# Kernel optimization log

Hardware: AMD Instinct MI355X
Metric: run time of the kernel (lower is better)

The kernel has to match this reference:

```python
import jax, jax.numpy as jnp
import numpy as np

N_P = 100000; N_F = 100000; N_PORT = 50000
F_IN = 64; H = 128; E = 200000; G = 128; OUT = 2


def setup_inputs() -> dict:
    key = jax.random.key(0)
    it = iter(jax.random.split(key, 64))
    def nrm(sh, s=1.0):
        return jax.random.normal(next(it), sh, jnp.float32) * s
    def ei(ns, nd):
        src = jax.random.randint(next(it), (E,), 0, ns)
        dst = jax.random.randint(next(it), (E,), 0, nd)
        return jnp.stack([src, dst]).astype(jnp.int32)
    def batch(n):
        return jnp.sort(jax.random.randint(next(it), (n,), 0, G)).astype(jnp.int32)
    return {
        'x_process': nrm((N_P, F_IN)), 'x_file': nrm((N_F, F_IN)), 'x_port': nrm((N_PORT, F_IN)),
        'W0': nrm((F_IN, H), 0.1), 'a0s': nrm((H,), 0.1), 'a0d': nrm((H,), 0.1), 'b0': jnp.zeros((H,), jnp.float32),
        'W1': nrm((H, H), 0.1), 'a1s': nrm((H,), 0.1), 'a1d': nrm((H,), 0.1), 'b1': jnp.zeros((H,), jnp.float32),
        'W2': nrm((H, H), 0.1), 'a2s': nrm((H,), 0.1), 'a2d': nrm((H,), 0.1), 'b2': jnp.zeros((H,), jnp.float32),
        'lin1_w': nrm((H, H), 0.1), 'lin1_b': jnp.zeros((H,), jnp.float32),
        'lin2_w': nrm((H, OUT), 0.1), 'lin2_b': jnp.zeros((OUT,), jnp.float32),
        'ei_access': ei(N_P, N_F), 'ei_rev_access': ei(N_F, N_P),
        'ei_same_as': ei(N_P, N_F), 'ei_rev_same_as': ei(N_F, N_P),
        'ei_bind': ei(N_P, N_PORT), 'ei_rev_bind': ei(N_PORT, N_P),
        'ei_session': ei(N_PORT, N_PORT), 'ei_rev_session': ei(N_PORT, N_PORT),
        'ei_create': ei(N_P, N_P), 'ei_rev_create': ei(N_P, N_P),
        'batch_process': batch(N_P), 'batch_file': batch(N_F), 'batch_port': batch(N_PORT),
    }


def _rel(h_src, s_src, d_dst, ei, b, n_dst):
    # single GATConv relation: gather, segment-softmax over dst, scatter-sum
    es, ed = ei[0], ei[1]
    alpha = jax.nn.leaky_relu(s_src[es] + d_dst[ed], 0.2)  # [E]
    m = jax.ops.segment_max(alpha, ed, num_segments=n_dst)
    m = jnp.where(jnp.isfinite(m), m, 0.0)
    ex = jnp.exp(alpha - m[ed])
    den = jax.ops.segment_sum(ex, ed, num_segments=n_dst)
    w = ex / jnp.maximum(den[ed], 1e-16)
    out = jax.ops.segment_sum(w[:, None] * h_src[es], ed, num_segments=n_dst)
    return out + b


def _forward(x_process, x_file, x_port,
             W0, a0s, a0d, b0, W1, a1s, a1d, b1, W2, a2s, a2d, b2,
             lin1_w, lin1_b, lin2_w, lin2_b,
             ei_access, ei_rev_access, ei_same_as, ei_rev_same_as,
             ei_bind, ei_rev_bind, ei_session, ei_rev_session,
             ei_create, ei_rev_create,
             batch_process, batch_file, batch_port):
    xp, xf, xpo = x_process, x_file, x_port
    for W, asr, adr, b in ((W0, a0s, a0d, b0), (W1, a1s, a1d, b1), (W2, a2s, a2d, b2)):
        # shared GATConv weights across all 10 relations -> transform each node type once
        hp, hf, hpo = xp @ W, xf @ W, xpo @ W
        sp, sf, spo = hp @ asr, hf @ asr, hpo @ asr
        dp, df, dpo = hp @ adr, hf @ adr, hpo @ adr
        # HeteroConv(aggr='mean'): average relation outputs per dst node type
        p_new = (_rel(hf, sf, dp, ei_rev_access, b, N_P)
                 + _rel(hf, sf, dp, ei_rev_same_as, b, N_P)
                 + _rel(hpo, spo, dp, ei_rev_bind, b, N_P)
                 + _rel(hp, sp, dp, ei_create, b, N_P)
                 + _rel(hp, sp, dp, ei_rev_create, b, N_P)) / 5.0
        f_new = (_rel(hp, sp, df, ei_access, b, N_F)
                 + _rel(hp, sp, df, ei_same_as, b, N_F)) / 2.0
        po_new = (_rel(hp, sp, dpo, ei_bind, b, N_PORT)
                  + _rel(hpo, spo, dpo, ei_session, b, N_PORT)
                  + _rel(hpo, spo, dpo, ei_rev_session, b, N_PORT)) / 3.0
        xp = jax.nn.leaky_relu(p_new, 0.01)
        xf = jax.nn.leaky_relu(f_new, 0.01)
        xpo = jax.nn.leaky_relu(po_new, 0.01)
    # pool_type == 1: global_add_pool over all node types concatenated
    x = jnp.concatenate([xp, xf, xpo], axis=0)
    bb = jnp.concatenate([batch_process, batch_file, batch_port], axis=0)
    pooled = jax.ops.segment_sum(x, bb, num_segments=G)  # [G, H]
    h = pooled @ lin1_w + lin1_b  # dropout is identity at eval
    return h @ lin2_w + lin2_b  # [G, OUT]


def reference(x_process, x_file, x_port,
              W0, a0s, a0d, b0, W1, a1s, a1d, b1, W2, a2s, a2d, b2,
              lin1_w, lin1_b, lin2_w, lin2_b,
              ei_access, ei_rev_access, ei_same_as, ei_rev_same_as,
              ei_bind, ei_rev_bind, ei_session, ei_rev_session,
              ei_create, ei_rev_create,
              batch_process, batch_file, batch_port):
    return _forward(x_process, x_file, x_port,
                    W0, a0s, a0d, b0, W1, a1s, a1d, b1, W2, a2s, a2d, b2,
                    lin1_w, lin1_b, lin2_w, lin2_b,
                    ei_access, ei_rev_access, ei_same_as, ei_rev_same_as,
                    ei_bind, ei_rev_bind, ei_session, ei_rev_session,
                    ei_create, ei_rev_create,
                    batch_process, batch_file, batch_port)
```

## Files before the change

kernel.cpp:

```cpp
#include <hip/hip_runtime.h>
#include <cstdint>
#include <cstddef>

#define E_EDGES 200000
#define NP 100000
#define NF 100000
#define NPORT 50000
#define NTOT 250000
#define TOTDEG 850000
#define GPOOL 128
#define NPART 8
#define SEGS_PER_PART 106250

typedef __attribute__((ext_vector_type(8))) short bf16x8;
typedef __attribute__((ext_vector_type(4))) float f32x4;

__device__ __forceinline__ float bf2f(unsigned short u) {
    return __uint_as_float(((unsigned int)u) << 16);
}
__device__ __forceinline__ unsigned short f2bf(float f) {
    unsigned int x = __float_as_uint(f);
    return (unsigned short)((x + 0x7fffu + ((x >> 16) & 1u)) >> 16);
}

struct EiPtrs {
    const int* p[10];
};

__device__ __forceinline__ int seg_of(int r, int dst) {
    if (r < 5) return dst * 5 + r;
    if (r < 7) return 500000 + dst * 2 + (r - 5);
    return 700000 + dst * 3 + (r - 7);
}
__device__ __forceinline__ int srcbase_of(int r) {
    return (r <= 1) ? 100000 : (r == 2 || r >= 8) ? 200000 : 0;
}

__global__ __launch_bounds__(256) void k_count_all(EiPtrs eis, int* __restrict__ deg) {
    int r = blockIdx.y;
    int e = blockIdx.x * 256 + threadIdx.x;
    if (e >= E_EDGES) return;
    int seg = seg_of(r, eis.p[r][E_EDGES + e]);
    int lo = blockIdx.z * SEGS_PER_PART;
    if (seg < lo || seg >= lo + SEGS_PER_PART) return;
    atomicAdd(&deg[seg], 1);
}

__global__ __launch_bounds__(256) void k_scan_partial(const int* __restrict__ deg,
                                                      int* __restrict__ bsum) {
    int t = threadIdx.x, b = blockIdx.x;
    int base = b * 1024 + t * 4;
    int sv = 0;
#pragma unroll
    for (int i = 0; i < 4; i++) {
        int idx = base + i;
        if (idx < TOTDEG) sv += deg[idx];
    }
#pragma unroll
    for (int msk = 1; msk < 64; msk <<= 1) sv += __shfl_xor(sv, msk);
    __shared__ int ws[4];
    if ((t & 63) == 0) ws[t >> 6] = sv;
    __syncthreads();
    if (t == 0) bsum[b] = ws[0] + ws[1] + ws[2] + ws[3];
}

__global__ __launch_bounds__(1024) void k_scan_bsums(int* __restrict__ bsum, int nb) {
    __shared__ int lds[1024];
    int t = threadIdx.x;
    int v = (t < nb) ? bsum[t] : 0;
    lds[t] = v;
    __syncthreads();
    for (int dd = 1; dd < 1024; dd <<= 1) {
        int u = (t >= dd) ? lds[t - dd] : 0;
        __syncthreads();
        lds[t] += u;
        __syncthreads();
    }
    if (t < nb) bsum[t] = lds[t] - v;
}

__global__ __launch_bounds__(256) void k_scan_final(const int* __restrict__ deg,
                                                    const int* __restrict__ bsum,
                                                    int* __restrict__ offs) {
    int t = threadIdx.x, b = blockIdx.x;
    int base = b * 1024 + t * 4;
    int v[4];
    int tot = 0;
#pragma unroll
    for (int i = 0; i < 4; i++) {
        int idx = base + i;
        v[i] = (idx < TOTDEG) ? deg[idx] : 0;
        tot += v[i];
    }
    int lane = t & 63, w = t >> 6;
    int x = tot;
#pragma unroll
    for (int dd = 1; dd < 64; dd <<= 1) {
        int u = __shfl_up(x, dd);
        if (lane >= dd) x += u;
    }
    __shared__ int wt[4];
    if (lane == 63) wt[w] = x;
    __syncthreads();
    int wbase = 0;
#pragma unroll
    for (int j = 0; j < 4; j++)
        if (j < w) wbase += wt[j];
    int run = bsum[b] + wbase + (x - tot);
#pragma unroll
    for (int i = 0; i < 4; i++) {
        int idx = base + i;
        if (idx <= TOTDEG) offs[idx] = run;
        run += v[i];
    }
}

__global__ __launch_bounds__(256) void k_fill_all(EiPtrs eis, int* __restrict__ cursor,
                                                  int* __restrict__ list) {
    int r = blockIdx.y;
    int e = blockIdx.x * 256 + threadIdx.x;
    if (e >= E_EDGES) return;
    const int* ei = eis.p[r];
    int seg = seg_of(r, ei[E_EDGES + e]);
    int lo = blockIdx.z * SEGS_PER_PART;
    if (seg < lo || seg >= lo + SEGS_PER_PART) return;
    int pos = atomicAdd(&cursor[seg], 1);
    list[pos] = ei[e] + srcbase_of(r);
}

__global__ __launch_bounds__(256) void k_wt(const float* __restrict__ W,
                                            unsigned short* __restrict__ WT, int K) {
    int idx = blockIdx.x * 256 + threadIdx.x;
    if (idx >= 128 * K) return;
    int col = idx / K, k = idx - col * K;
    WT[idx] = f2bf(W[k * 128 + col]);
}

template <int K, bool BF16IN>
__global__ __launch_bounds__(256) void gemm_mfma(const void* __restrict__ xv,
                                                 const unsigned short* __restrict__ WT,
                                                 const float* __restrict__ avs,
                                                 const float* __restrict__ avd,
                                                 unsigned short* __restrict__ h,
                                                 float* __restrict__ s,
                                                 float* __restrict__ d, int N) {
    constexpr int NQ = K / 32;
    __shared__ float csmem[64][130];
    char* sw = (char*)&csmem[0][0];
    int tid = threadIdx.x;
    int w = tid >> 6, l = tid & 63;
    int row0 = blockIdx.x * 64;

    constexpr int WT_BYTES = 128 * K * 2;
#pragma unroll
    for (int i = tid * 16; i < WT_BYTES; i += 256 * 16) {
        uint4 v = *(const uint4*)((const char*)WT + i);
        int row = i / (2 * K);
        int addr = i ^ ((row & 7) << 4);
        *(uint4*)(sw + addr) = v;
    }

    int arow = row0 + w * 16 + (l & 15);
    bf16x8 afrag[NQ];
    if (arow < N) {
        if (BF16IN) {
            const unsigned short* x = (const unsigned short*)xv;
#pragma unroll
            for (int q = 0; q < NQ; ++q) {
                int kc = q * 32 + (l >> 4) * 8;
                afrag[q] = *(const bf16x8*)&x[(size_t)arow * K + kc];
            }
        } else {
            const float* x = (const float*)xv;
#pragma unroll
            for (int q = 0; q < NQ; ++q) {
                int kc = q * 32 + (l >> 4) * 8;
                float4 f0 = *(const float4*)&x[(size_t)arow * K + kc];
                float4 f1 = *(const float4*)&x[(size_t)arow * K + kc + 4];
                bf16x8 a;
                a[0] = (short)f2bf(f0.x);
                a[1] = (short)f2bf(f0.y);
                a[2] = (short)f2bf(f0.z);
                a[3] = (short)f2bf(f0.w);
                a[4] = (short)f2bf(f1.x);
                a[5] = (short)f2bf(f1.y);
                a[6] = (short)f2bf(f1.z);
                a[7] = (short)f2bf(f1.w);
                afrag[q] = a;
            }
        }
    } else {
#pragma unroll
        for (int q = 0; q < NQ; ++q) {
            bf16x8 z = {0, 0, 0, 0, 0, 0, 0, 0};
            afrag[q] = z;
        }
    }
    __syncthreads();

    f32x4 acc[8];
#pragma unroll
    for (int c = 0; c < 8; ++c) acc[c] = (f32x4){0.f, 0.f, 0.f, 0.f};

#pragma unroll
    for (int c = 0; c < 8; ++c) {
        int cabs = c * 16 + (l & 15);
        int base = cabs * (2 * K) + ((l >> 4) * 16);
        int swz = (cabs & 7) << 4;
#pragma unroll
        for (int q = 0; q < NQ; ++q) {
            int addr = (base + q * 64) ^ swz;
            bf16x8 b = *(const bf16x8*)(sw + addr);
            acc[c] = __builtin_amdgcn_mfma_f32_16x16x32_bf16(afrag[q], b, acc[c], 0, 0, 0);
        }
    }
    __syncthreads();

    int crow = w * 16 + (l >> 4) * 4;
    int ccol = l & 15;
#pragma unroll
    for (int c = 0; c < 8; ++c)
#pragma unroll
        for (int r = 0; r < 4; ++r) csmem[crow + r][c * 16 + ccol] = acc[c][r];
    __syncthreads();

    int row = tid >> 2, cg = tid & 3;
    int grow = row0 + row;
    if (grow < N) {
        float sv = 0.f, dv = 0.f;
        unsigned short tmp[32];
#pragma unroll
        for (int i = 0; i < 32; ++i) {
            float v = csmem[row][cg * 32 + i];
            sv = fmaf(v, avs[cg * 32 + i], sv);
            dv = fmaf(v, avd[cg * 32 + i], dv);
            tmp[i] = f2bf(v);
        }
        unsigned short* hp = &h[(size_t)grow * 128 + cg * 32];
        *(uint4*)&hp[0] = *(uint4*)&tmp[0];
        *(uint4*)&hp[8] = *(uint4*)&tmp[8];
        *(uint4*)&hp[16] = *(uint4*)&tmp[16];
        *(uint4*)&hp[24] = *(uint4*)&tmp[24];
        sv += __shfl_xor(sv, 1);
        sv += __shfl_xor(sv, 2);
        dv += __shfl_xor(dv, 1);
        dv += __shfl_xor(dv, 2);
        if (cg == 0) {
            s[grow] = sv;
            d[grow] = dv;
        }
    }
}

__global__ __launch_bounds__(256) void k_edgew(const int* __restrict__ offs,
                                               const int* __restrict__ list,
                                               const float* __restrict__ s_all,
                                               const float* __restrict__ d_all,
                                               unsigned short* __restrict__ wE) {
    int seg = blockIdx.x * 256 + threadIdx.x;
    if (seg >= TOTDEG) return;
    int o0 = offs[seg], o1 = offs[seg + 1];
    if (o1 == o0) return;
    int dst_g;
    if (seg < 500000)
        dst_g = seg / 5;
    else if (seg < 700000)
        dst_g = 100000 + (seg - 500000) / 2;
    else
        dst_g = 200000 + (seg - 700000) / 3;
    float dd = d_all[dst_g];
    float m = -1e30f, den = 0.f;
    for (int j = o0; j < o1; ++j) {
        float x = s_all[list[j]] + dd;
        x = (x >= 0.f) ? x : 0.2f * x;
        if (x > m) {
            den = den * __expf(m - x) + 1.f;
            m = x;
        } else {
            den += __expf(x - m);
        }
    }
    float invden = 1.f / fmaxf(den, 1e-16f);
    for (int j = o0; j < o1; ++j) {
        float x = s_all[list[j]] + dd;
        x = (x >= 0.f) ? x : 0.2f * x;
        wE[j] = f2bf(__expf(x - m) * invden);
    }
}

__global__ __launch_bounds__(256) void k_gather(const int* __restrict__ offs,
                                                const int* __restrict__ list,
                                                const unsigned short* __restrict__ wE,
                                                const float* __restrict__ bias,
                                                const unsigned short* __restrict__ H,
                                                unsigned short* __restrict__ X) {
    int grp = threadIdx.x >> 5, lane = threadIdx.x & 31;
    int dst = blockIdx.x * 8 + grp;
    if (dst >= NTOT) return;
    int seg0, nrel;
    float inv;
    if (dst < 100000) {
        seg0 = dst * 5;
        nrel = 5;
        inv = 0.2f;
    } else if (dst < 200000) {
        seg0 = 500000 + (dst - 100000) * 2;
        nrel = 2;
        inv = 0.5f;
    } else {
        seg0 = 700000 + (dst - 200000) * 3;
        nrel = 3;
        inv = 1.f / 3.f;
    }
    int o0 = offs[seg0], o1 = offs[seg0 + nrel];
    int half = lane >> 4;
    int l16 = lane & 15;
    float a[8] = {0.f, 0.f, 0.f, 0.f, 0.f, 0.f, 0.f, 0.f};
    float b[8] = {0.f, 0.f, 0.f, 0.f, 0.f, 0.f, 0.f, 0.f};
    int j = o0 + half;
    for (; j + 2 < o1; j += 4) {
        int s0 = list[j], s1 = list[j + 2];
        float w0 = bf2f(wE[j]), w1 = bf2f(wE[j + 2]);
        uint4 r0 = *(const uint4*)&H[(size_t)s0 * 128 + l16 * 8];
        uint4 r1 = *(const uint4*)&H[(size_t)s1 * 128 + l16 * 8];
        const unsigned short* u0 = (const unsigned short*)&r0;
        const unsigned short* u1 = (const unsigned short*)&r1;
#pragma unroll
        for (int k = 0; k < 8; ++k) a[k] = fmaf(w0, bf2f(u0[k]), a[k]);
#pragma unroll
        for (int k = 0; k < 8; ++k) b[k] = fmaf(w1, bf2f(u1[k]), b[k]);
    }
    for (; j < o1; j += 2) {
        int s0 = list[j];
        float w0 = bf2f(wE[j]);
        uint4 r0 = *(const uint4*)&H[(size_t)s0 * 128 + l16 * 8];
        const unsigned short* u0 = (const unsigned short*)&r0;
#pragma unroll
        for (int k = 0; k < 8; ++k) a[k] = fmaf(w0, bf2f(u0[k]), a[k]);
    }
#pragma unroll
    for (int k = 0; k < 8; ++k) {
        a[k] += b[k];
        a[k] += __shfl_xor(a[k], 16);
    }
    int c0 = l16 * 8 + half * 4;
    float4 b4 = *(const float4*)&bias[c0];
    float v0 = fmaf(a[half * 4 + 0], inv, b4.x);
    float v1 = fmaf(a[half * 4 + 1], inv, b4.y);
    float v2 = fmaf(a[half * 4 + 2], inv, b4.z);
    float v3 = fmaf(a[half * 4 + 3], inv, b4.w);
    v0 = (v0 >= 0.f) ? v0 : 0.01f * v0;
    v1 = (v1 >= 0.f) ? v1 : 0.01f * v1;
    v2 = (v2 >= 0.f) ? v2 : 0.01f * v2;
    v3 = (v3 >= 0.f) ? v3 : 0.01f * v3;
    ushort4 o;
    o.x = f2bf(v0);
    o.y = f2bf(v1);
    o.z = f2bf(v2);
    o.w = f2bf(v3);
    *(ushort4*)&X[(size_t)dst * 128 + c0] = o;
}

__global__ __launch_bounds__(128) void pool_all(const unsigned short* __restrict__ X,
                                                const int* __restrict__ bp,
                                                const int* __restrict__ bf,
                                                const int* __restrict__ bpo,
                                                float* __restrict__ pooled) {
    int t = threadIdx.x;
    int start = blockIdx.x * 128;
    int end = min(start + 128, NTOT);
    if (start >= end) return;
    auto bat = [&](int i) {
        return (i < NP) ? bp[i] : (i < NP + NF) ? bf[i - NP] : bpo[i - NP - NF];
    };
    float acc = 0.f;
    int g = bat(start);
    for (int i = start; i < end; ++i) {
        int gi = bat(i);
        if (gi != g) {
            atomicAdd(&pooled[(size_t)g * 128 + t], acc);
            acc = 0.f;
            g = gi;
        }
        acc += bf2f(X[(size_t)i * 128 + t]);
    }
    atomicAdd(&pooled[(size_t)g * 128 + t], acc);
}

__global__ __launch_bounds__(128) void k_mlp(const float* __restrict__ pooled,
                                             const float* __restrict__ w1,
                                             const float* __restrict__ b1,
                                             const float* __restrict__ w2,
                                             const float* __restrict__ b2,
                                             float* __restrict__ out) {
    __shared__ float p[128];
    __shared__ float r0[2], r1[2];
    int g = blockIdx.x, t = threadIdx.x;
    p[t] = pooled[g * 128 + t];
    __syncthreads();
    float acc = b1[t];
    for (int k = 0; k < 128; ++k) acc = fmaf(p[k], w1[k * 128 + t], acc);
    float v0 = acc * w2[t * 2 + 0];
    float v1 = acc * w2[t * 2 + 1];
#pragma unroll
    for (int msk = 1; msk < 64; msk <<= 1) {
        v0 += __shfl_xor(v0, msk);
        v1 += __shfl_xor(v1, msk);
    }
    if ((t & 63) == 0) {
        r0[t >> 6] = v0;
        r1[t >> 6] = v1;
    }
    __syncthreads();
    if (t == 0) {
        out[g * 2 + 0] = r0[0] + r0[1] + b2[0];
        out[g * 2 + 1] = r1[0] + r1[1] + b2[1];
    }
}

__global__ void k_ws_debug(float* out, int n, float val) {
    int i = blockIdx.x * 256 + threadIdx.x;
    if (i < n) out[i] = val;
}

extern "C" void kernel_launch(void* const* d_in, const int* in_sizes, int n_in,
                              void* d_out, int out_size, void* d_ws, size_t ws_size,
                              hipStream_t stream) {
    const float* x_p0 = (const float*)d_in[0];
    const float* x_f0 = (const float*)d_in[1];
    const float* x_po0 = (const float*)d_in[2];
    const float* Wl[3] = {(const float*)d_in[3], (const float*)d_in[7],
                          (const float*)d_in[11]};
    const float* asl[3] = {(const float*)d_in[4], (const float*)d_in[8],
                           (const float*)d_in[12]};
    const float* adl[3] = {(const float*)d_in[5], (const float*)d_in[9],
                           (const float*)d_in[13]};
    const float* bl[3] = {(const float*)d_in[6], (const float*)d_in[10],
                          (const float*)d_in[14]};
    const float* lin1_w = (const float*)d_in[15];
    const float* lin1_b = (const float*)d_in[16];
    const float* lin2_w = (const float*)d_in[17];
    const float* lin2_b = (const float*)d_in[18];
    EiPtrs eis;
    eis.p[0] = (const int*)d_in[20];
    eis.p[1] = (const int*)d_in[22];
    eis.p[2] = (const int*)d_in[24];
    eis.p[3] = (const int*)d_in[27];
    eis.p[4] = (const int*)d_in[28];
    eis.p[5] = (const int*)d_in[19];
    eis.p[6] = (const int*)d_in[21];
    eis.p[7] = (const int*)d_in[23];
    eis.p[8] = (const int*)d_in[25];
    eis.p[9] = (const int*)d_in[26];
    const int* batch_p = (const int*)d_in[29];
    const int* batch_f = (const int*)d_in[30];
    const int* batch_po = (const int*)d_in[31];
    float* out = (float*)d_out;

    char* w = (char*)d_ws;
    size_t off = 0;
    int* offs = (int*)(w + off);      off += (size_t)850004 * 4;
    int* cursor = (int*)(w + off);    off += (size_t)TOTDEG * 4;
    int* list = (int*)(w + off);      off += (size_t)10 * E_EDGES * 4;
    int* bsum = (int*)(w + off);      off += 4096;
    unsigned short* H = (unsigned short*)(w + off); off += (size_t)NTOT * 128 * 2;
    unsigned short* X = (unsigned short*)(w + off); off += (size_t)NTOT * 128 * 2;
    float* s_all = (float*)(w + off); off += (size_t)NTOT * 4;
    float* d_all = (float*)(w + off); off += (size_t)NTOT * 4;
    float* pooled = (float*)(w + off); off += (size_t)GPOOL * 128 * 4;
    unsigned short* WT0 = (unsigned short*)(w + off); off += (size_t)128 * 64 * 2;
    unsigned short* WT1 = (unsigned short*)(w + off); off += (size_t)128 * 128 * 2;
    unsigned short* WT2 = (unsigned short*)(w + off); off += (size_t)128 * 128 * 2;
    unsigned short* wE = (unsigned short*)(w + off); off += (size_t)10 * E_EDGES * 2;
    if (ws_size < off) {
        k_ws_debug<<<(out_size + 255) / 256, 256, 0, stream>>>(out, out_size,
                                                               (float)ws_size);
        return;
    }

    hipMemsetAsync(cursor, 0, (size_t)TOTDEG * 4, stream);
    hipMemsetAsync(pooled, 0, (size_t)GPOOL * 128 * 4, stream);

    k_wt<<<(128 * 64 + 255) / 256, 256, 0, stream>>>(Wl[0], WT0, 64);
    k_wt<<<(128 * 128 + 255) / 256, 256, 0, stream>>>(Wl[1], WT1, 128);
    k_wt<<<(128 * 128 + 255) / 256, 256, 0, stream>>>(Wl[2], WT2, 128);

    int eb = (E_EDGES + 255) / 256;
    k_count_all<<<dim3(eb, 10, NPART), 256, 0, stream>>>(eis, cursor);
    int nb = (TOTDEG + 1 + 1023) / 1024;
    k_scan_partial<<<nb, 256, 0, stream>>>(cursor, bsum);
    k_scan_bsums<<<1, 1024, 0, stream>>>(bsum, nb);
    k_scan_final<<<nb, 256, 0, stream>>>(cursor, bsum, offs);
    hipMemcpyAsync(cursor, offs, (size_t)TOTDEG * 4, hipMemcpyDeviceToDevice, stream);
    k_fill_all<<<dim3(eb, 10, NPART), 256, 0, stream>>>(eis, cursor, list);

    unsigned short* Hp = H;
    unsigned short* Hf = H + (size_t)NP * 128;
    unsigned short* Hpo = H + (size_t)(NP + NF) * 128;
    float* sp_ = s_all;
    float* sf_ = s_all + NP;
    float* spo_ = s_all + NP + NF;
    float* dp_ = d_all;
    float* df_ = d_all + NP;
    float* dpo_ = d_all + NP + NF;

    for (int L = 0; L < 3; ++L) {
        if (L == 0) {
            gemm_mfma<64, false><<<(NP + 63) / 64, 256, 0, stream>>>(
                x_p0, WT0, asl[0], adl[0], Hp, sp_, dp_, NP);
            gemm_mfma<64, false><<<(NF + 63) / 64, 256, 0, stream>>>(
                x_f0, WT0, asl[0], adl[0], Hf, sf_, df_, NF);
            gemm_mfma<64, false><<<(NPORT + 63) / 64, 256, 0, stream>>>(
                x_po0, WT0, asl[0], adl[0], Hpo, spo_, dpo_, NPORT);
        } else {
            const unsigned short* WTL = (L == 1) ? WT1 : WT2;
            gemm_mfma<128, true><<<(NTOT + 63) / 64, 256, 0, stream>>>(
                X, WTL, asl[L], adl[L], H, s_all, d_all, NTOT);
        }
        k_edgew<<<(TOTDEG + 255) / 256, 256, 0, stream>>>(offs, list, s_all, d_all, wE);
        k_gather<<<(NTOT + 7) / 8, 256, 0, stream>>>(offs, list, wE, bl[L], H, X);
    }

    pool_all<<<(NTOT + 127) / 128, 128, 0, stream>>>(X, batch_p, batch_f, batch_po,
                                                     pooled);

    k_mlp<<<GPOOL, 128, 0, stream>>>(pooled, lin1_w, lin1_b, lin2_w, lin2_b, out);
}
```

Before: 862.8 us.

## Fuse edge softmax into gather, merge init kernels and layer-0 GEMM launches

```diff
diff --git a/kernel.cpp b/kernel.cpp
--- a/kernel.cpp
+++ b/kernel.cpp
@@ -9,8 +9,11 @@
 #define NTOT 250000
 #define TOTDEG 850000
 #define GPOOL 128
-#define NPART 8
-#define SEGS_PER_PART 106250
+#define NPART_C 2
+#define SPP_C 425000
+#define NPART_F 4
+#define SPP_F 212500
+#define CAPW 128
 
 typedef __attribute__((ext_vector_type(8))) short bf16x8;
 typedef __attribute__((ext_vector_type(4))) float f32x4;
@@ -34,6 +37,28 @@
 }
 __device__ __forceinline__ int srcbase_of(int r) {
     return (r <= 1) ? 100000 : (r == 2 || r >= 8) ? 200000 : 0;
+}
+
+__global__ __launch_bounds__(256) void k_init(const float* __restrict__ W0,
+                                              const float* __restrict__ W1,
+                                              const float* __restrict__ W2,
+                                              unsigned short* __restrict__ WT0,
+                                              unsigned short* __restrict__ WT1,
+                                              unsigned short* __restrict__ WT2,
+                                              int* __restrict__ cursor,
+                                              float* __restrict__ pooled) {
+    int idx = blockIdx.x * 256 + threadIdx.x;
+    if (idx < TOTDEG) cursor[idx] = 0;
+    if (idx < GPOOL * 128) pooled[idx] = 0.f;
+    if (idx < 128 * 64) {
+        int col = idx / 64, k = idx - col * 64;
+        WT0[idx] = f2bf(W0[k * 128 + col]);
+    }
+    if (idx < 128 * 128) {
+        int col = idx >> 7, k = idx & 127;
+        WT1[idx] = f2bf(W1[k * 128 + col]);
+        WT2[idx] = f2bf(W2[k * 128 + col]);
+    }
 }
 
 __global__ __launch_bounds__(256) void k_count_all(EiPtrs eis, int* __restrict__ deg) {
@@ -41,8 +66,8 @@
     int e = blockIdx.x * 256 + threadIdx.x;
     if (e >= E_EDGES) return;
     int seg = seg_of(r, eis.p[r][E_EDGES + e]);
-    int lo = blockIdx.z * SEGS_PER_PART;
-    if (seg < lo || seg >= lo + SEGS_PER_PART) return;
+    int lo = blockIdx.z * SPP_C;
+    if (seg < lo || seg >= lo + SPP_C) return;
     atomicAdd(&deg[seg], 1);
 }
 
@@ -81,7 +106,8 @@
 
 __global__ __launch_bounds__(256) void k_scan_final(const int* __restrict__ deg,
                                                     const int* __restrict__ bsum,
-                                                    int* __restrict__ offs) {
+                                                    int* __restrict__ offs,
+                                                    int* __restrict__ cursor) {
     int t = threadIdx.x, b = blockIdx.x;
     int base = b * 1024 + t * 4;
     int v[4];
@@ -111,6 +137,7 @@
     for (int i = 0; i < 4; i++) {
         int idx = base + i;
         if (idx <= TOTDEG) offs[idx] = run;
+        if (idx < TOTDEG) cursor[idx] = run;
         run += v[i];
     }
 }
@@ -122,34 +149,25 @@
     if (e >= E_EDGES) return;
     const int* ei = eis.p[r];
     int seg = seg_of(r, ei[E_EDGES + e]);
-    int lo = blockIdx.z * SEGS_PER_PART;
-    if (seg < lo || seg >= lo + SEGS_PER_PART) return;
+    int lo = blockIdx.z * SPP_F;
+    if (seg < lo || seg >= lo + SPP_F) return;
     int pos = atomicAdd(&cursor[seg], 1);
     list[pos] = ei[e] + srcbase_of(r);
 }
 
-__global__ __launch_bounds__(256) void k_wt(const float* __restrict__ W,
-                                            unsigned short* __restrict__ WT, int K) {
-    int idx = blockIdx.x * 256 + threadIdx.x;
-    if (idx >= 128 * K) return;
-    int col = idx / K, k = idx - col * K;
-    WT[idx] = f2bf(W[k * 128 + col]);
-}
-
 template <int K, bool BF16IN>
-__global__ __launch_bounds__(256) void gemm_mfma(const void* __restrict__ xv,
-                                                 const unsigned short* __restrict__ WT,
-                                                 const float* __restrict__ avs,
-                                                 const float* __restrict__ avd,
-                                                 unsigned short* __restrict__ h,
-                                                 float* __restrict__ s,
-                                                 float* __restrict__ d, int N) {
+__device__ __forceinline__ void gemm_body(const void* __restrict__ xv,
+                                          const unsigned short* __restrict__ WT,
+                                          const float* __restrict__ avs,
+                                          const float* __restrict__ avd,
+                                          unsigned short* __restrict__ h,
+                                          float* __restrict__ s, float* __restrict__ d,
+                                          int N, int row0) {
     constexpr int NQ = K / 32;
     __shared__ float csmem[64][130];
     char* sw = (char*)&csmem[0][0];
     int tid = threadIdx.x;
     int w = tid >> 6, l = tid & 63;
-    int row0 = blockIdx.x * 64;
 
     constexpr int WT_BYTES = 128 * K * 2;
 #pragma unroll
@@ -252,91 +270,147 @@
     }
 }
 
-__global__ __launch_bounds__(256) void k_edgew(const int* __restrict__ offs,
-                                               const int* __restrict__ list,
-                                               const float* __restrict__ s_all,
-                                               const float* __restrict__ d_all,
-                                               unsigned short* __restrict__ wE) {
-    int seg = blockIdx.x * 256 + threadIdx.x;
-    if (seg >= TOTDEG) return;
-    int o0 = offs[seg], o1 = offs[seg + 1];
-    if (o1 == o0) return;
-    int dst_g;
-    if (seg < 500000)
-        dst_g = seg / 5;
-    else if (seg < 700000)
-        dst_g = 100000 + (seg - 500000) / 2;
-    else
-        dst_g = 200000 + (seg - 700000) / 3;
-    float dd = d_all[dst_g];
-    float m = -1e30f, den = 0.f;
-    for (int j = o0; j < o1; ++j) {
-        float x = s_all[list[j]] + dd;
-        x = (x >= 0.f) ? x : 0.2f * x;
-        if (x > m) {
-            den = den * __expf(m - x) + 1.f;
-            m = x;
-        } else {
-            den += __expf(x - m);
-        }
-    }
-    float invden = 1.f / fmaxf(den, 1e-16f);
-    for (int j = o0; j < o1; ++j) {
-        float x = s_all[list[j]] + dd;
-        x = (x >= 0.f) ? x : 0.2f * x;
-        wE[j] = f2bf(__expf(x - m) * invden);
-    }
-}
-
-__global__ __launch_bounds__(256) void k_gather(const int* __restrict__ offs,
-                                                const int* __restrict__ list,
-                                                const unsigned short* __restrict__ wE,
-                                                const float* __restrict__ bias,
-                                                const unsigned short* __restrict__ H,
-                                                unsigned short* __restrict__ X) {
-    int grp = threadIdx.x >> 5, lane = threadIdx.x & 31;
-    int dst = blockIdx.x * 8 + grp;
-    if (dst >= NTOT) return;
-    int seg0, nrel;
-    float inv;
-    if (dst < 100000) {
-        seg0 = dst * 5;
-        nrel = 5;
-        inv = 0.2f;
-    } else if (dst < 200000) {
-        seg0 = 500000 + (dst - 100000) * 2;
-        nrel = 2;
-        inv = 0.5f;
+__global__ __launch_bounds__(256) void gemm_l0(const float* __restrict__ xp,
+                                               const float* __restrict__ xf,
+                                               const float* __restrict__ xpo,
+                                               const unsigned short* __restrict__ WT,
+                                               const float* __restrict__ avs,
+                                               const float* __restrict__ avd,
+                                               unsigned short* __restrict__ H,
+                                               float* __restrict__ s_all,
+                                               float* __restrict__ d_all) {
+    int ty = blockIdx.y;
+    const float* x;
+    int N, rowoff;
+    if (ty == 0) {
+        x = xp;
+        N = NP;
+        rowoff = 0;
+    } else if (ty == 1) {
+        x = xf;
+        N = NF;
+        rowoff = NP;
     } else {
-        seg0 = 700000 + (dst - 200000) * 3;
-        nrel = 3;
-        inv = 1.f / 3.f;
-    }
-    int o0 = offs[seg0], o1 = offs[seg0 + nrel];
-    int half = lane >> 4;
-    int l16 = lane & 15;
+        x = xpo;
+        N = NPORT;
+        rowoff = NP + NF;
+    }
+    int row0 = blockIdx.x * 64;
+    if (row0 >= N) return;
+    gemm_body<64, false>(x, WT, avs, avd, H + (size_t)rowoff * 128, s_all + rowoff,
+                         d_all + rowoff, N, row0);
+}
+
+__global__ __launch_bounds__(256) void gemm_big(const unsigned short* __restrict__ X,
+                                                const unsigned short* __restrict__ WT,
+                                                const float* __restrict__ avs,
+                                                const float* __restrict__ avd,
+                                                unsigned short* __restrict__ H,
+                                                float* __restrict__ s_all,
+                                                float* __restrict__ d_all) {
+    gemm_body<128, true>(X, WT, avs, avd, H, s_all, d_all, NTOT, blockIdx.x * 64);
+}
+
+template <int NREL>
+__device__ float slow_w(int j, const int* o, float dd, const int* __restrict__ list,
+                        const float* __restrict__ s_all) {
+    float w = 0.f;
+#pragma unroll
+    for (int r = 0; r < NREL; ++r) {
+        if (j >= o[r] && j < o[r + 1]) {
+            float m = -1e30f, den = 0.f;
+            for (int k = o[r]; k < o[r + 1]; ++k) {
+                float x = s_all[list[k]] + dd;
+                x = (x >= 0.f) ? x : 0.2f * x;
+                if (x > m) {
+                    den = den * __expf(m - x) + 1.f;
+                    m = x;
+                } else {
+                    den += __expf(x - m);
+                }
+            }
+            float xj = s_all[list[j]] + dd;
+            xj = (xj >= 0.f) ? xj : 0.2f * xj;
+            w = __expf(xj - m) / fmaxf(den, 1e-16f);
+        }
+    }
+    return w;
+}
+
+template <int NREL>
+__device__ __forceinline__ void gather_one(int dst, int seg0, float inv_nrel, int lane,
+                                           const int* __restrict__ offs,
+                                           const int* __restrict__ list,
+                                           const float* __restrict__ s_all,
+                                           const float* __restrict__ d_all,
+                                           const float* __restrict__ bias,
+                                           const unsigned short* __restrict__ H,
+                                           unsigned short* __restrict__ X,
+                                           float* __restrict__ wl) {
+    int o[NREL + 1];
+#pragma unroll
+    for (int i = 0; i <= NREL; ++i) o[i] = offs[seg0 + i];
+    const int base = o[0], oend = o[NREL];
+    const float dd = d_all[dst];
+#pragma unroll
+    for (int r = 0; r < NREL; ++r) {
+        int s = o[r], e = o[r + 1];
+        if (e <= s) continue;
+        float m = -1e30f, den = 0.f;
+        for (int j = s; j < e; ++j) {
+            float x = s_all[list[j]] + dd;
+            x = (x >= 0.f) ? x : 0.2f * x;
+            if (x > m) {
+                den = den * __expf(m - x) + 1.f;
+                m = x;
+            } else {
+                den += __expf(x - m);
+            }
+        }
+        float invd = 1.f / fmaxf(den, 1e-16f);
+        for (int j = s + lane; j < e; j += 32) {
+            float x = s_all[list[j]] + dd;
+            x = (x >= 0.f) ? x : 0.2f * x;
+            int idx = j - base;
+            if (idx < CAPW) wl[idx] = __expf(x - m) * invd;
+        }
+    }
+    __builtin_amdgcn_wave_barrier();
+
+    int half = lane >> 4, l16 = lane & 15;
     float a[8] = {0.f, 0.f, 0.f, 0.f, 0.f, 0.f, 0.f, 0.f};
     float b[8] = {0.f, 0.f, 0.f, 0.f, 0.f, 0.f, 0.f, 0.f};
-    int j = o0 + half;
-    for (; j + 2 < o1; j += 4) {
-        int s0 = list[j], s1 = list[j + 2];
-        float w0 = bf2f(wE[j]), w1 = bf2f(wE[j + 2]);
-        uint4 r0 = *(const uint4*)&H[(size_t)s0 * 128 + l16 * 8];
-        uint4 r1 = *(const uint4*)&H[(size_t)s1 * 128 + l16 * 8];
-        const unsigned short* u0 = (const unsigned short*)&r0;
-        const unsigned short* u1 = (const unsigned short*)&r1;
-#pragma unroll
-        for (int k = 0; k < 8; ++k) a[k] = fmaf(w0, bf2f(u0[k]), a[k]);
-#pragma unroll
-        for (int k = 0; k < 8; ++k) b[k] = fmaf(w1, bf2f(u1[k]), b[k]);
-    }
-    for (; j < o1; j += 2) {
-        int s0 = list[j];
-        float w0 = bf2f(wE[j]);
-        uint4 r0 = *(const uint4*)&H[(size_t)s0 * 128 + l16 * 8];
-        const unsigned short* u0 = (const unsigned short*)&r0;
-#pragma unroll
-        for (int k = 0; k < 8; ++k) a[k] = fmaf(w0, bf2f(u0[k]), a[k]);
+    if (oend - base <= CAPW) {
+        int j = base + half;
+        for (; j + 2 < oend; j += 4) {
+            int s0 = list[j], s1 = list[j + 2];
+            float w0 = wl[j - base], w1 = wl[j + 2 - base];
+            uint4 r0 = *(const uint4*)&H[(size_t)s0 * 128 + l16 * 8];
+            uint4 r1 = *(const uint4*)&H[(size_t)s1 * 128 + l16 * 8];
+            const unsigned short* u0 = (const unsigned short*)&r0;
+            const unsigned short* u1 = (const unsigned short*)&r1;
+#pragma unroll
+            for (int k = 0; k < 8; ++k) a[k] = fmaf(w0, bf2f(u0[k]), a[k]);
+#pragma unroll
+            for (int k = 0; k < 8; ++k) b[k] = fmaf(w1, bf2f(u1[k]), b[k]);
+        }
+        for (; j < oend; j += 2) {
+            int s0 = list[j];
+            float w0 = wl[j - base];
+            uint4 r0 = *(const uint4*)&H[(size_t)s0 * 128 + l16 * 8];
+            const unsigned short* u0 = (const unsigned short*)&r0;
+#pragma unroll
+            for (int k = 0; k < 8; ++k) a[k] = fmaf(w0, bf2f(u0[k]), a[k]);
+        }
+    } else {
+        for (int j = base + half; j < oend; j += 2) {
+            int s0 = list[j];
+            float w0 = slow_w<NREL>(j, o, dd, list, s_all);
+            uint4 r0 = *(const uint4*)&H[(size_t)s0 * 128 + l16 * 8];
+            const unsigned short* u0 = (const unsigned short*)&r0;
+#pragma unroll
+            for (int k = 0; k < 8; ++k) a[k] = fmaf(w0, bf2f(u0[k]), a[k]);
+        }
     }
 #pragma unroll
     for (int k = 0; k < 8; ++k) {
@@ -345,20 +419,42 @@
     }
     int c0 = l16 * 8 + half * 4;
     float4 b4 = *(const float4*)&bias[c0];
-    float v0 = fmaf(a[half * 4 + 0], inv, b4.x);
-    float v1 = fmaf(a[half * 4 + 1], inv, b4.y);
-    float v2 = fmaf(a[half * 4 + 2], inv, b4.z);
-    float v3 = fmaf(a[half * 4 + 3], inv, b4.w);
+    float v0 = fmaf(a[half * 4 + 0], inv_nrel, b4.x);
+    float v1 = fmaf(a[half * 4 + 1], inv_nrel, b4.y);
+    float v2 = fmaf(a[half * 4 + 2], inv_nrel, b4.z);
+    float v3 = fmaf(a[half * 4 + 3], inv_nrel, b4.w);
     v0 = (v0 >= 0.f) ? v0 : 0.01f * v0;
     v1 = (v1 >= 0.f) ? v1 : 0.01f * v1;
     v2 = (v2 >= 0.f) ? v2 : 0.01f * v2;
     v3 = (v3 >= 0.f) ? v3 : 0.01f * v3;
-    ushort4 o;
-    o.x = f2bf(v0);
-    o.y = f2bf(v1);
-    o.z = f2bf(v2);
-    o.w = f2bf(v3);
-    *(ushort4*)&X[(size_t)dst * 128 + c0] = o;
+    ushort4 ov;
+    ov.x = f2bf(v0);
+    ov.y = f2bf(v1);
+    ov.z = f2bf(v2);
+    ov.w = f2bf(v3);
+    *(ushort4*)&X[(size_t)dst * 128 + c0] = ov;
+}
+
+__global__ __launch_bounds__(256) void k_gather(const int* __restrict__ offs,
+                                                const int* __restrict__ list,
+                                                const float* __restrict__ s_all,
+                                                const float* __restrict__ d_all,
+                                                const float* __restrict__ bias,
+                                                const unsigned short* __restrict__ H,
+                                                unsigned short* __restrict__ X) {
+    __shared__ float wlds[8][CAPW];
+    int grp = threadIdx.x >> 5, lane = threadIdx.x & 31;
+    int dst = blockIdx.x * 8 + grp;
+    if (dst >= NTOT) return;
+    float* wl = wlds[grp];
+    if (dst < NP)
+        gather_one<5>(dst, dst * 5, 0.2f, lane, offs, list, s_all, d_all, bias, H, X, wl);
+    else if (dst < NP + NF)
+        gather_one<2>(dst, 500000 + (dst - NP) * 2, 0.5f, lane, offs, list, s_all, d_all,
+                      bias, H, X, wl);
+    else
+        gather_one<3>(dst, 700000 + (dst - NP - NF) * 3, 1.f / 3.f, lane, offs, list,
+                      s_all, d_all, bias, H, X, wl);
 }
 
 __global__ __launch_bounds__(128) void pool_all(const unsigned short* __restrict__ X,
@@ -471,54 +567,34 @@
     unsigned short* WT0 = (unsigned short*)(w + off); off += (size_t)128 * 64 * 2;
     unsigned short* WT1 = (unsigned short*)(w + off); off += (size_t)128 * 128 * 2;
     unsigned short* WT2 = (unsigned short*)(w + off); off += (size_t)128 * 128 * 2;
-    unsigned short* wE = (unsigned short*)(w + off); off += (size_t)10 * E_EDGES * 2;
     if (ws_size < off) {
         k_ws_debug<<<(out_size + 255) / 256, 256, 0, stream>>>(out, out_size,
                                                                (float)ws_size);
         return;
     }
 
-    hipMemsetAsync(cursor, 0, (size_t)TOTDEG * 4, stream);
-    hipMemsetAsync(pooled, 0, (size_t)GPOOL * 128 * 4, stream);
-
-    k_wt<<<(128 * 64 + 255) / 256, 256, 0, stream>>>(Wl[0], WT0, 64);
-    k_wt<<<(128 * 128 + 255) / 256, 256, 0, stream>>>(Wl[1], WT1, 128);
-    k_wt<<<(128 * 128 + 255) / 256, 256, 0, stream>>>(Wl[2], WT2, 128);
+    k_init<<<(TOTDEG + 255) / 256, 256, 0, stream>>>(Wl[0], Wl[1], Wl[2], WT0, WT1, WT2,
+                                                     cursor, pooled);
 
     int eb = (E_EDGES + 255) / 256;
-    k_count_all<<<dim3(eb, 10, NPART), 256, 0, stream>>>(eis, cursor);
+    k_count_all<<<dim3(eb, 10, NPART_C), 256, 0, stream>>>(eis, cursor);
     int nb = (TOTDEG + 1 + 1023) / 1024;
     k_scan_partial<<<nb, 256, 0, stream>>>(cursor, bsum);
     k_scan_bsums<<<1, 1024, 0, stream>>>(bsum, nb);
-    k_scan_final<<<nb, 256, 0, stream>>>(cursor, bsum, offs);
-    hipMemcpyAsync(cursor, offs, (size_t)TOTDEG * 4, hipMemcpyDeviceToDevice, stream);
-    k_fill_all<<<dim3(eb, 10, NPART), 256, 0, stream>>>(eis, cursor, list);
-
-    unsigned short* Hp = H;
-    unsigned short* Hf = H + (size_t)NP * 128;
-    unsigned short* Hpo = H + (size_t)(NP + NF) * 128;
-    float* sp_ = s_all;
-    float* sf_ = s_all + NP;
-    float* spo_ = s_all + NP + NF;
-    float* dp_ = d_all;
-    float* df_ = d_all + NP;
-    float* dpo_ = d_all + NP + NF;
+    k_scan_final<<<nb, 256, 0, stream>>>(cursor, bsum, offs, cursor);
+    k_fill_all<<<dim3(eb, 10, NPART_F), 256, 0, stream>>>(eis, cursor, list);
 
     for (int L = 0; L < 3; ++L) {
         if (L == 0) {
-            gemm_mfma<64, false><<<(NP + 63) / 64, 256, 0, stream>>>(
-                x_p0, WT0, asl[0], adl[0], Hp, sp_, dp_, NP);
-            gemm_mfma<64, false><<<(NF + 63) / 64, 256, 0, stream>>>(
-                x_f0, WT0, asl[0], adl[0], Hf, sf_, df_, NF);
-            gemm_mfma<64, false><<<(NPORT + 63) / 64, 256, 0, stream>>>(
-                x_po0, WT0, asl[0], adl[0], Hpo, spo_, dpo_, NPORT);
+            gemm_l0<<<dim3((NP + 63) / 64, 3), 256, 0, stream>>>(
+                x_p0, x_f0, x_po0, WT0, asl[0], adl[0], H, s_all, d_all);
         } else {
             const unsigned short* WTL = (L == 1) ? WT1 : WT2;
-            gemm_mfma<128, true><<<(NTOT + 63) / 64, 256, 0, stream>>>(
-                X, WTL, asl[L], adl[L], H, s_all, d_all, NTOT);
-        }
-        k_edgew<<<(TOTDEG + 255) / 256, 256, 0, stream>>>(offs, list, s_all, d_all, wE);
-        k_gather<<<(NTOT + 7) / 8, 256, 0, stream>>>(offs, list, wE, bl[L], H, X);
+            gemm_big<<<(NTOT + 63) / 64, 256, 0, stream>>>(X, WTL, asl[L], adl[L], H,
+                                                           s_all, d_all);
+        }
+        k_gather<<<(NTOT + 7) / 8, 256, 0, stream>>>(offs, list, s_all, d_all, bl[L], H,
+                                                     X);
     }
 
     pool_all<<<(NTOT + 127) / 128, 128, 0, stream>>>(X, batch_p, batch_f, batch_po,
```

Measured after the change: 1.149 ms. +33.1%, slower.

## Merge setup kernels, fuse cursor copy into scan, batch layer-0 GEMMs

Applied to the files above, without the earlier changes.

```diff
diff --git a/kernel.cpp b/kernel.cpp
--- a/kernel.cpp
+++ b/kernel.cpp
@@ -9,8 +9,10 @@
 #define NTOT 250000
 #define TOTDEG 850000
 #define GPOOL 128
-#define NPART 8
-#define SEGS_PER_PART 106250
+#define NPART_C 2
+#define SPP_C 425000
+#define NPART_F 4
+#define SPP_F 212500
 
 typedef __attribute__((ext_vector_type(8))) short bf16x8;
 typedef __attribute__((ext_vector_type(4))) float f32x4;
@@ -34,6 +36,28 @@
 }
 __device__ __forceinline__ int srcbase_of(int r) {
     return (r <= 1) ? 100000 : (r == 2 || r >= 8) ? 200000 : 0;
+}
+
+__global__ __launch_bounds__(256) void k_init(const float* __restrict__ W0,
+                                              const float* __restrict__ W1,
+                                              const float* __restrict__ W2,
+                                              unsigned short* __restrict__ WT0,
+                                              unsigned short* __restrict__ WT1,
+                                              unsigned short* __restrict__ WT2,
+                                              int* __restrict__ cursor,
+                                              float* __restrict__ pooled) {
+    int idx = blockIdx.x * 256 + threadIdx.x;
+    if (idx < TOTDEG) cursor[idx] = 0;
+    if (idx < GPOOL * 128) pooled[idx] = 0.f;
+    if (idx < 128 * 64) {
+        int col = idx / 64, k = idx - col * 64;
+        WT0[idx] = f2bf(W0[k * 128 + col]);
+    }
+    if (idx < 128 * 128) {
+        int col = idx >> 7, k = idx & 127;
+        WT1[idx] = f2bf(W1[k * 128 + col]);
+        WT2[idx] = f2bf(W2[k * 128 + col]);
+    }
 }
 
 __global__ __launch_bounds__(256) void k_count_all(EiPtrs eis, int* __restrict__ deg) {
@@ -41,8 +65,8 @@
     int e = blockIdx.x * 256 + threadIdx.x;
     if (e >= E_EDGES) return;
     int seg = seg_of(r, eis.p[r][E_EDGES + e]);
-    int lo = blockIdx.z * SEGS_PER_PART;
-    if (seg < lo || seg >= lo + SEGS_PER_PART) return;
+    int lo = blockIdx.z * SPP_C;
+    if (seg < lo || seg >= lo + SPP_C) return;
     atomicAdd(&deg[seg], 1);
 }
 
@@ -81,7 +105,8 @@
 
 __global__ __launch_bounds__(256) void k_scan_final(const int* __restrict__ deg,
                                                     const int* __restrict__ bsum,
-                                                    int* __restrict__ offs) {
+                                                    int* __restrict__ offs,
+                                                    int* __restrict__ cursor) {
     int t = threadIdx.x, b = blockIdx.x;
     int base = b * 1024 + t * 4;
     int v[4];
@@ -111,6 +136,7 @@
     for (int i = 0; i < 4; i++) {
         int idx = base + i;
         if (idx <= TOTDEG) offs[idx] = run;
+        if (idx < TOTDEG) cursor[idx] = run;
         run += v[i];
     }
 }
@@ -122,34 +148,25 @@
     if (e >= E_EDGES) return;
     const int* ei = eis.p[r];
     int seg = seg_of(r, ei[E_EDGES + e]);
-    int lo = blockIdx.z * SEGS_PER_PART;
-    if (seg < lo || seg >= lo + SEGS_PER_PART) return;
+    int lo = blockIdx.z * SPP_F;
+    if (seg < lo || seg >= lo + SPP_F) return;
     int pos = atomicAdd(&cursor[seg], 1);
     list[pos] = ei[e] + srcbase_of(r);
 }
 
-__global__ __launch_bounds__(256) void k_wt(const float* __restrict__ W,
-                                            unsigned short* __restrict__ WT, int K) {
-    int idx = blockIdx.x * 256 + threadIdx.x;
-    if (idx >= 128 * K) return;
-    int col = idx / K, k = idx - col * K;
-    WT[idx] = f2bf(W[k * 128 + col]);
-}
-
 template <int K, bool BF16IN>
-__global__ __launch_bounds__(256) void gemm_mfma(const void* __restrict__ xv,
-                                                 const unsigned short* __restrict__ WT,
-                                                 const float* __restrict__ avs,
-                                                 const float* __restrict__ avd,
-                                                 unsigned short* __restrict__ h,
-                                                 float* __restrict__ s,
-                                                 float* __restrict__ d, int N) {
+__device__ __forceinline__ void gemm_body(const void* __restrict__ xv,
+                                          const unsigned short* __restrict__ WT,
+                                          const float* __restrict__ avs,
+                                          const float* __restrict__ avd,
+                                          unsigned short* __restrict__ h,
+                                          float* __restrict__ s, float* __restrict__ d,
+                                          int N, int row0) {
     constexpr int NQ = K / 32;
     __shared__ float csmem[64][130];
     char* sw = (char*)&csmem[0][0];
     int tid = threadIdx.x;
     int w = tid >> 6, l = tid & 63;
-    int row0 = blockIdx.x * 64;
 
     constexpr int WT_BYTES = 128 * K * 2;
 #pragma unroll
@@ -250,6 +267,47 @@
             d[grow] = dv;
         }
     }
+}
+
+__global__ __launch_bounds__(256) void gemm_l0(const float* __restrict__ xp,
+                                               const float* __restrict__ xf,
+                                               const float* __restrict__ xpo,
+                                               const unsigned short* __restrict__ WT,
+                                               const float* __restrict__ avs,
+                                               const float* __restrict__ avd,
+                                               unsigned short* __restrict__ H,
+                                               float* __restrict__ s_all,
+                                               float* __restrict__ d_all) {
+    int ty = blockIdx.y;
+    const float* x;
+    int N, rowoff;
+    if (ty == 0) {
+        x = xp;
+        N = NP;
+        rowoff = 0;
+    } else if (ty == 1) {
+        x = xf;
+        N = NF;
+        rowoff = NP;
+    } else {
+        x = xpo;
+        N = NPORT;
+        rowoff = NP + NF;
+    }
+    int row0 = blockIdx.x * 64;
+    if (row0 >= N) return;
+    gemm_body<64, false>(x, WT, avs, avd, H + (size_t)rowoff * 128, s_all + rowoff,
+                         d_all + rowoff, N, row0);
+}
+
+__global__ __launch_bounds__(256) void gemm_big(const unsigned short* __restrict__ X,
+                                                const unsigned short* __restrict__ WT,
+                                                const float* __restrict__ avs,
+                                                const float* __restrict__ avd,
+                                                unsigned short* __restrict__ H,
+                                                float* __restrict__ s_all,
+                                                float* __restrict__ d_all) {
+    gemm_body<128, true>(X, WT, avs, avd, H, s_all, d_all, NTOT, blockIdx.x * 64);
 }
 
 __global__ __launch_bounds__(256) void k_edgew(const int* __restrict__ offs,
@@ -478,44 +536,25 @@
         return;
     }
 
-    hipMemsetAsync(cursor, 0, (size_t)TOTDEG * 4, stream);
-    hipMemsetAsync(pooled, 0, (size_t)GPOOL * 128 * 4, stream);
-
-    k_wt<<<(128 * 64 + 255) / 256, 256, 0, stream>>>(Wl[0], WT0, 64);
-    k_wt<<<(128 * 128 + 255) / 256, 256, 0, stream>>>(Wl[1], WT1, 128);
-    k_wt<<<(128 * 128 + 255) / 256, 256, 0, stream>>>(Wl[2], WT2, 128);
+    k_init<<<(TOTDEG + 255) / 256, 256, 0, stream>>>(Wl[0], Wl[1], Wl[2], WT0, WT1, WT2,
+                                                     cursor, pooled);
 
     int eb = (E_EDGES + 255) / 256;
-    k_count_all<<<dim3(eb, 10, NPART), 256, 0, stream>>>(eis, cursor);
+    k_count_all<<<dim3(eb, 10, NPART_C), 256, 0, stream>>>(eis, cursor);
     int nb = (TOTDEG + 1 + 1023) / 1024;
     k_scan_partial<<<nb, 256, 0, stream>>>(cursor, bsum);
     k_scan_bsums<<<1, 1024, 0, stream>>>(bsum, nb);
-    k_scan_final<<<nb, 256, 0, stream>>>(cursor, bsum, offs);
-    hipMemcpyAsync(cursor, offs, (size_t)TOTDEG * 4, hipMemcpyDeviceToDevice, stream);
-    k_fill_all<<<dim3(eb, 10, NPART), 256, 0, stream>>>(eis, cursor, list);
-
-    unsigned short* Hp = H;
-    unsigned short* Hf = H + (size_t)NP * 128;
-    unsigned short* Hpo = H + (size_t)(NP + NF) * 128;
-    float* sp_ = s_all;
-    float* sf_ = s_all + NP;
-    float* spo_ = s_all + NP + NF;
-    float* dp_ = d_all;
-    float* df_ = d_all + NP;
-    float* dpo_ = d_all + NP + NF;
+    k_scan_final<<<nb, 256, 0, stream>>>(cursor, bsum, offs, cursor);
+    k_fill_all<<<dim3(eb, 10, NPART_F), 256, 0, stream>>>(eis, cursor, list);
 
     for (int L = 0; L < 3; ++L) {
         if (L == 0) {
-            gemm_mfma<64, false><<<(NP + 63) / 64, 256, 0, stream>>>(
-                x_p0, WT0, asl[0], adl[0], Hp, sp_, dp_, NP);
-            gemm_mfma<64, false><<<(NF + 63) / 64, 256, 0, stream>>>(
-                x_f0, WT0, asl[0], adl[0], Hf, sf_, df_, NF);
-            gemm_mfma<64, false><<<(NPORT + 63) / 64, 256, 0, stream>>>(
-                x_po0, WT0, asl[0], adl[0], Hpo, spo_, dpo_, NPORT);
+            gemm_l0<<<dim3((NP + 63) / 64, 3), 256, 0, stream>>>(
+                x_p0, x_f0, x_po0, WT0, asl[0], adl[0], H, s_all, d_all);
         } else {
             const unsigned short* WTL = (L == 1) ? WT1 : WT2;
-            gemm_mfma<128, true><<<(NTOT + 63) / 64, 256, 0, stream>>>(
-                X, WTL, asl[L], adl[L], H, s_all, d_all, NTOT);
+            gemm_big<<<(NTOT + 63) / 64, 256, 0, stream>>>(X, WTL, asl[L], adl[L], H,
+                                                           s_all, d_all);
         }
         k_edgew<<<(TOTDEG + 255) / 256, 256, 0, stream>>>(offs, list, s_all, d_all, wE);
         k_gather<<<(NTOT + 7) / 8, 256, 0, stream>>>(offs, list, wE, bl[L], H, X);
```

Measured after the change: 861.3 us. Within noise of the previous version (-0.2%).
